# Performance work log

Hardware: AMD Instinct MI355X
Metric: run time of the kernel (lower is better)

The kernel has to match this reference:

```python
import jax, jax.numpy as jnp
import numpy as np
from jax import lax

B, T, H, W, D = 4, 24, 32, 32, 128
N_CONV = 5            # 32 -> 1 via five stride-2 convs
NUM_FREQS = T // 2    # 12
N_EXPERTS = 7         # unique int periods of rfftfreq(24)[1:]
TOP_K = 2
BN_EPS = 1e-5
COMBINE_EPS = float(np.finfo(np.float64).eps)


def setup_inputs() -> dict:
    key = jax.random.key(0)
    ks = jax.random.split(key, 12)
    x = jax.random.normal(ks[0], (B, T, H, W, D), jnp.float32)
    conv_w = jax.random.normal(ks[1], (N_CONV, D, D, 2, 2), jnp.float32) / np.sqrt(4 * D)
    conv_b = jax.random.normal(ks[2], (N_CONV, D), jnp.float32) * 0.1
    bn_gamma = jax.random.uniform(ks[3], (N_CONV, D), jnp.float32, 0.5, 1.5)
    bn_beta = jax.random.normal(ks[4], (N_CONV, D), jnp.float32) * 0.1
    bn_mean = jax.random.normal(ks[5], (N_CONV, D), jnp.float32) * 0.1
    bn_var = jax.random.uniform(ks[6], (N_CONV, D), jnp.float32, 0.5, 1.5)
    fuse_w = jax.random.normal(ks[7], (D, 1), jnp.float32) / np.sqrt(D)
    fuse_b = jax.random.normal(ks[8], (1,), jnp.float32) * 0.1
    w_gate = jax.random.normal(ks[9], (NUM_FREQS, N_EXPERTS), jnp.float32)
    expert_w = jax.random.normal(ks[10], (N_EXPERTS, D, D), jnp.float32) / np.sqrt(D)
    expert_b = jax.random.normal(ks[11], (N_EXPERTS, D), jnp.float32) * 0.1
    return dict(x=x, conv_w=conv_w, conv_b=conv_b, bn_gamma=bn_gamma, bn_beta=bn_beta,
                bn_mean=bn_mean, bn_var=bn_var, fuse_w=fuse_w, fuse_b=fuse_b,
                w_gate=w_gate, expert_w=expert_w, expert_b=expert_b, top_k=TOP_K)


def _gates(x, conv_w, conv_b, bn_gamma, bn_beta, bn_mean, bn_var, fuse_w, fuse_b, w_gate, top_k):
    b, t, h, w, d = x.shape
    # (b t h w d) -> (bt, d, h, w)
    z = jnp.transpose(x.reshape(b * t, h, w, d), (0, 3, 1, 2))
    for i in range(conv_w.shape[0]):  # fixed small layer loop
        z = lax.conv_general_dilated(z, conv_w[i], (2, 2), 'VALID',
                                     dimension_numbers=('NCHW', 'OIHW', 'NCHW'))
        z = z + conv_b[i][None, :, None, None]
        z = bn_gamma[i][None, :, None, None] * (z - bn_mean[i][None, :, None, None]) \
            * lax.rsqrt(bn_var[i][None, :, None, None] + BN_EPS) + bn_beta[i][None, :, None, None]
        z = jnp.where(z > 0, z, 0.2 * z)  # LeakyReLU(0.2)
    hh, ww = z.shape[-2], z.shape[-1]
    # (bt, d, h, w) -> (b, t, h*w*d)  matching einops '(b t) d h w -> b t (h w d)'
    z = jnp.transpose(z.reshape(b, t, d, hh, ww), (0, 1, 3, 4, 2)).reshape(b, t, hh * ww * d)
    s = (z @ fuse_w + fuse_b)[..., 0]  # [B, T]
    xf = jnp.fft.rfft(s, axis=-1, norm='ortho')[:, 1:]  # drop DC -> [B, T//2]
    amp = jnp.abs(xf)
    logits = amp @ w_gate  # [B, E]  (eval path: no noise)
    top_vals, top_idx = lax.top_k(logits, top_k + 1)
    tk_vals, tk_idx = top_vals[:, :top_k], top_idx[:, :top_k]
    tk_gates = jax.nn.softmax(tk_vals, axis=-1)
    gates = jnp.zeros_like(logits).at[jnp.arange(b)[:, None], tk_idx].set(tk_gates)
    return gates


def reference(x, conv_w, conv_b, bn_gamma, bn_beta, bn_mean, bn_var,
              fuse_w, fuse_b, w_gate, expert_w, expert_b, top_k):
    gates = _gates(x, conv_w, conv_b, bn_gamma, bn_beta, bn_mean, bn_var,
                   fuse_w, fuse_b, w_gate, top_k)  # [B, E]
    # Dense equivalent of dispatch -> per-expert linear -> combine:
    # combine does exp(expert_out), gate-weighted scatter-add over batch, then log.
    expert_out = jnp.einsum('bthwd,edf->bethwf', x, expert_w) \
                 + expert_b[None, :, None, None, None, :]  # [B,E,T,H,W,D]
    combined = jnp.einsum('be,bethwf->bthwf', gates, jnp.exp(expert_out))
    combined = jnp.where(combined == 0, COMBINE_EPS, combined)
    return jnp.log(combined)
```

## Files before the change

### kernel.cpp

```cpp
#include <hip/hip_runtime.h>
#include <hip/hip_bf16.h>

#define D_ 128
#define T_ 24
#define NPB 24576
#define TSTR 132

typedef __attribute__((ext_vector_type(8))) short bf16x8;
typedef __attribute__((ext_vector_type(4))) float f32x4;
typedef unsigned short ushortt;

static __device__ __forceinline__ void load8(const float* p, float* dst){
  float4 a = *(const float4*)p; float4 b = *(const float4*)(p+4);
  dst[0]=a.x;dst[1]=a.y;dst[2]=a.z;dst[3]=a.w;dst[4]=b.x;dst[5]=b.y;dst[6]=b.z;dst[7]=b.w;
}
static __device__ __forceinline__ bf16x8 cvt8(const float* f){
  union { bf16x8 v; __hip_bfloat162 h[4]; } u;
#pragma unroll
  for (int i=0;i<4;i++) u.h[i] = __float22bfloat162_rn(make_float2(f[2*i], f[2*i+1]));
  return u.v;
}
static __device__ __forceinline__ void split8(const float* f, bf16x8* hh, bf16x8* ll){
  union { bf16x8 v; __hip_bfloat162 h[4]; } uh, ul;
  float lo[8];
#pragma unroll
  for (int i=0;i<4;i++){
    __hip_bfloat162 p = __float22bfloat162_rn(make_float2(f[2*i], f[2*i+1]));
    uh.h[i] = p;
    lo[2*i]   = f[2*i]   - __bfloat162float(p.x);
    lo[2*i+1] = f[2*i+1] - __bfloat162float(p.y);
  }
#pragma unroll
  for (int i=0;i<4;i++) ul.h[i] = __float22bfloat162_rn(make_float2(lo[2*i], lo[2*i+1]));
  *hh = uh.v; *ll = ul.v;
}

__global__ void prep_frags(const float* __restrict__ cw, const float* __restrict__ ew,
                           ushortt* __restrict__ wfC, ushortt* __restrict__ wfE, int do_e)
{
  const int idx = blockIdx.x*256 + threadIdx.x;
  if (idx < 10240){
    const int l  = idx >> 11;
    const int n  = (idx >> 4) & 127;
    const int k8 = (idx & 15) * 8;
    const float* src = cw + (size_t)((l*128 + n)*128 + k8)*4;
    float4 v[8];
#pragma unroll
    for (int kk=0;kk<8;++kk) v[kk] = *(const float4*)&src[kk*4];
    const int fk = k8>>5, q = (k8>>3)&3, ng = n>>4;
    const int lanoff = (q*16 + (n&15))*8;
#pragma unroll
    for (int tap=0; tap<4; ++tap){
      float f[8];
#pragma unroll
      for (int kk=0;kk<8;++kk) f[kk] = ((const float*)&v[kk])[tap];
      bf16x8 hh, ll; split8(f, &hh, &ll);
      *(bf16x8*)&wfC[(size_t)((((l*4+tap)*2+0)*4+fk)*8+ng)*512 + lanoff] = hh;
      *(bf16x8*)&wfC[(size_t)((((l*4+tap)*2+1)*4+fk)*8+ng)*512 + lanoff] = ll;
    }
  } else if (do_e && idx < 10240 + 14336){
    const int j  = idx - 10240;
    const int e  = j >> 11;
    const int n  = (j >> 4) & 127;
    const int k8 = (j & 15) * 8;
    float f[8];
#pragma unroll
    for (int kk=0;kk<8;++kk) f[kk] = ew[(size_t)(e*128 + k8+kk)*128 + n];
    const int fk = k8>>5, q = (k8>>3)&3, ng = n>>4;
    *(bf16x8*)&wfE[(size_t)((e*4+fk)*8+ng)*512 + (q*16 + (n&15))*8] = cvt8(f);
  }
}

template<int MG>
__global__ __launch_bounds__(256, 4)
void conv3(const float* __restrict__ in, float* __restrict__ out,
           const ushortt* __restrict__ wf,
           const float* __restrict__ cb,  const float* __restrict__ gam,
           const float* __restrict__ bet, const float* __restrict__ mn,
           const float* __restrict__ vr,  int n_pix, int lw)
{
  (void)n_pix;
  const int t = threadIdx.x;
  const int w = t>>6, lane = t&63, quad = lane>>4, l16 = lane&15;
  const int nh = w*32;
  const int row0 = blockIdx.x*(MG*16);
  const int Win = 2<<lw;
  int inb[MG];
#pragma unroll
  for (int mg=0; mg<MG; ++mg){
    const int p = row0 + mg*16 + l16;
    const int n   = p >> (2*lw);
    const int rem = p - (n << (2*lw));
    const int oy  = rem >> lw, ox = rem - (oy<<lw);
    inb[mg] = ((n*Win  + 2*oy)*Win + 2*ox) << 7;
  }
  f32x4 acc[MG][2];
#pragma unroll
  for (int mg=0;mg<MG;++mg){ acc[mg][0]=(f32x4){0,0,0,0}; acc[mg][1]=acc[mg][0]; }

#pragma unroll
  for (int tap=0; tap<4; ++tap){
    const int toff = (((tap>>1)*Win) + (tap&1)) << 7;
#pragma unroll
    for (int fk=0; fk<4; ++fk){
      bf16x8 ah[MG], al[MG];
#pragma unroll
      for (int mg=0; mg<MG; ++mg){
        float f[8]; load8(in + inb[mg] + toff + fk*32 + quad*8, f);
        split8(f, &ah[mg], &al[mg]);
      }
#pragma unroll
      for (int ngl=0; ngl<2; ++ngl){
        const int ng = w*2 + ngl;
        const bf16x8 bh = *(const bf16x8*)&wf[(size_t)(((tap*2+0)*4+fk)*8+ng)*512 + lane*8];
        const bf16x8 bl = *(const bf16x8*)&wf[(size_t)(((tap*2+1)*4+fk)*8+ng)*512 + lane*8];
#pragma unroll
        for (int mg=0; mg<MG; ++mg){
          acc[mg][ngl] = __builtin_amdgcn_mfma_f32_16x16x32_bf16(ah[mg], bh, acc[mg][ngl], 0,0,0);
          acc[mg][ngl] = __builtin_amdgcn_mfma_f32_16x16x32_bf16(ah[mg], bl, acc[mg][ngl], 0,0,0);
          acc[mg][ngl] = __builtin_amdgcn_mfma_f32_16x16x32_bf16(al[mg], bh, acc[mg][ngl], 0,0,0);
        }
      }
    }
  }
#pragma unroll
  for (int ngl=0; ngl<2; ++ngl){
    const int col = nh + ngl*16 + l16;
    const float sc  = gam[col]*rsqrtf(vr[col]+1e-5f);
    const float cbv = cb[col], bt = bet[col], mv = mn[col];
#pragma unroll
    for (int mg=0; mg<MG; ++mg)
#pragma unroll
      for (int r=0; r<4; ++r){
        const int pix = row0 + mg*16 + quad*4 + r;
        float v = acc[mg][ngl][r] + cbv;
        v = sc*(v - mv) + bt;
        out[(size_t)pix*D_ + col] = v>0.f ? v : 0.2f*v;
      }
  }
}

template<int WOUT>
static __device__ __forceinline__ void stage_lds(const float* __restrict__ sIn,
    float* __restrict__ sOut, float* __restrict__ gOut,
    const ushortt* __restrict__ wf,
    const float* __restrict__ cb, const float* __restrict__ gam,
    const float* __restrict__ bet, const float* __restrict__ mn,
    const float* __restrict__ vr, int t)
{
  const int w = t>>6, lane = t&63, quad = lane>>4, l16 = lane&15;
  const int nh = w*32;
  const int R  = WOUT*WOUT;
  const int Wi = 2*WOUT;
  const int p  = (l16 < R) ? l16 : 0;
  const int oy = (WOUT==4) ? (p>>2) : (WOUT==2 ? (p>>1) : 0);
  const int ox = (WOUT==4) ? (p&3)  : (WOUT==2 ? (p&1)  : 0);
  const int inb = 2*oy*Wi + 2*ox;
  f32x4 acc[2];
  acc[0]=(f32x4){0,0,0,0}; acc[1]=acc[0];
#pragma unroll
  for (int tap=0; tap<4; ++tap){
    const int toff = (tap>>1)*Wi + (tap&1);
#pragma unroll
    for (int fk=0; fk<4; ++fk){
      float f[8]; load8(sIn + (size_t)(inb+toff)*TSTR + fk*32 + quad*8, f);
      bf16x8 ah, al; split8(f, &ah, &al);
#pragma unroll
      for (int ngl=0; ngl<2; ++ngl){
        const int ng = w*2 + ngl;
        const bf16x8 bh = *(const bf16x8*)&wf[(size_t)(((tap*2+0)*4+fk)*8+ng)*512 + lane*8];
        const bf16x8 bl = *(const bf16x8*)&wf[(size_t)(((tap*2+1)*4+fk)*8+ng)*512 + lane*8];
        acc[ngl] = __builtin_amdgcn_mfma_f32_16x16x32_bf16(ah, bh, acc[ngl], 0,0,0);
        acc[ngl] = __builtin_amdgcn_mfma_f32_16x16x32_bf16(ah, bl, acc[ngl], 0,0,0);
        acc[ngl] = __builtin_amdgcn_mfma_f32_16x16x32_bf16(al, bh, acc[ngl], 0,0,0);
      }
    }
  }
#pragma unroll
  for (int ngl=0; ngl<2; ++ngl){
    const int col = nh + ngl*16 + l16;
    const float sc  = gam[col]*rsqrtf(vr[col]+1e-5f);
    const float cbv = cb[col], btv = bet[col], mv = mn[col];
#pragma unroll
    for (int r=0; r<4; ++r){
      const int row = quad*4 + r;
      if (row < R){
        float v = acc[ngl][r] + cbv;
        v = sc*(v - mv) + btv;
        v = v>0.f ? v : 0.2f*v;
        if (WOUT > 1) sOut[(size_t)row*TSTR + col] = v;
        else          gOut[col] = v;
      }
    }
  }
}

__global__ __launch_bounds__(256, 2)
void tail_kernel(const float* __restrict__ bufA, const ushortt* __restrict__ wfC,
                 const float* __restrict__ cb,  const float* __restrict__ gam,
                 const float* __restrict__ bet, const float* __restrict__ mn,
                 const float* __restrict__ vr,  float* __restrict__ zbuf)
{
  __shared__ float sA[64*TSTR];
  __shared__ float sB[16*TSTR];
  __shared__ float sC[ 4*TSTR];
  const int bt = blockIdx.x;
  const int t = threadIdx.x;
  const int w = t>>6, lane = t&63, quad = lane>>4, l16 = lane&15;
  const int nh = w*32;

  {
    const ushortt* wf = wfC + 131072;
    int inb[4];
#pragma unroll
    for (int mg=0; mg<4; ++mg){
      const int p = mg*16 + l16;
      const int oy = p>>3, ox = p&7;
      inb[mg] = ((bt*16 + 2*oy)*16 + 2*ox) << 7;
    }
    f32x4 acc[4][2];
#pragma unroll
    for (int mg=0;mg<4;++mg){ acc[mg][0]=(f32x4){0,0,0,0}; acc[mg][1]=acc[mg][0]; }
#pragma unroll
    for (int tap=0; tap<4; ++tap){
      const int toff = (((tap>>1)*16) + (tap&1)) << 7;
#pragma unroll
      for (int fk=0; fk<4; ++fk){
        bf16x8 ah[4], al[4];
#pragma unroll
        for (int mg=0; mg<4; ++mg){
          float f[8]; load8(bufA + (size_t)inb[mg] + toff + fk*32 + quad*8, f);
          split8(f, &ah[mg], &al[mg]);
        }
#pragma unroll
        for (int ngl=0; ngl<2; ++ngl){
          const int ng = w*2 + ngl;
          const bf16x8 bh = *(const bf16x8*)&wf[(size_t)(((tap*2+0)*4+fk)*8+ng)*512 + lane*8];
          const bf16x8 bl = *(const bf16x8*)&wf[(size_t)(((tap*2+1)*4+fk)*8+ng)*512 + lane*8];
#pragma unroll
          for (int mg=0; mg<4; ++mg){
            acc[mg][ngl] = __builtin_amdgcn_mfma_f32_16x16x32_bf16(ah[mg], bh, acc[mg][ngl], 0,0,0);
            acc[mg][ngl] = __builtin_amdgcn_mfma_f32_16x16x32_bf16(ah[mg], bl, acc[mg][ngl], 0,0,0);
            acc[mg][ngl] = __builtin_amdgcn_mfma_f32_16x16x32_bf16(al[mg], bh, acc[mg][ngl], 0,0,0);
          }
        }
      }
    }
#pragma unroll
    for (int ngl=0; ngl<2; ++ngl){
      const int col = nh + ngl*16 + l16;
      const float sc  = gam[128+col]*rsqrtf(vr[128+col]+1e-5f);
      const float cbv = cb[128+col], btv = bet[128+col], mv = mn[128+col];
#pragma unroll
      for (int mg=0; mg<4; ++mg)
#pragma unroll
        for (int r=0; r<4; ++r){
          const int row = mg*16 + quad*4 + r;
          float v = acc[mg][ngl][r] + cbv;
          v = sc*(v - mv) + btv;
          sA[(size_t)row*TSTR + col] = v>0.f ? v : 0.2f*v;
        }
    }
  }
  __syncthreads();
  stage_lds<4>(sA, sB, nullptr, wfC + 262144, cb+256, gam+256, bet+256, mn+256, vr+256, t);
  __syncthreads();
  stage_lds<2>(sB, sC, nullptr, wfC + 393216, cb+384, gam+384, bet+384, mn+384, vr+384, t);
  __syncthreads();
  stage_lds<1>(sC, nullptr, zbuf + (size_t)bt*D_, wfC + 524288, cb+512, gam+512, bet+512, mn+512, vr+512, t);
}

__global__ void gate_kernel(const float* __restrict__ z, const float* __restrict__ fw,
                            const float* __restrict__ fb, const float* __restrict__ wg,
                            float* __restrict__ gbuf)
{
  __shared__ float s[96];
  __shared__ float amp[4][12];
  __shared__ float logits[4][7];
  const int t = threadIdx.x;
  if (t < 96){
    float a = 0.f;
    for (int d=0; d<D_; d++) a = fmaf(z[t*D_+d], fw[d], a);
    s[t] = a + fb[0];
  }
  __syncthreads();
  if (t < 48){
    const int b = t / 12, kf = (t % 12) + 1;
    float re=0.f, im=0.f;
    for (int tt=0; tt<T_; tt++){
      int ph = (kf*tt) % T_;
      float ang = (float)ph * (6.283185307179586f / (float)T_);
      re = fmaf(s[b*T_+tt], cosf(ang), re);
      im = fmaf(s[b*T_+tt], sinf(ang), im);
    }
    amp[b][t%12] = sqrtf(re*re + im*im) * 0.20412414523193150f;
  }
  __syncthreads();
  if (t < 28){
    const int b = t/7, e = t - (t/7)*7;
    float a = 0.f;
    for (int k=0;k<12;k++) a = fmaf(amp[b][k], wg[k*7+e], a);
    logits[b][e] = a;
  }
  __syncthreads();
  if (t < 4){
    const int b = t;
    int i0=0; float v0=logits[b][0];
    for (int e=1;e<7;e++){ float v=logits[b][e]; if (v > v0){ v0=v; i0=e; } }
    int i1=-1; float v1=-3.4e38f;
    for (int e=0;e<7;e++){ if (e==i0) continue; float v=logits[b][e]; if (v > v1){ v1=v; i1=e; } }
    float ed = expf(v1 - v0);
    gbuf[b*4+0] = 1.f/(1.f+ed);
    gbuf[b*4+1] = ed/(1.f+ed);
    ((int*)gbuf)[b*4+2] = i0;
    ((int*)gbuf)[b*4+3] = i1;
  }
}

__global__ __launch_bounds__(256, 3)
void expert_gate(const float* __restrict__ x, const ushortt* __restrict__ wfe,
                 const float* __restrict__ eb, const float* __restrict__ zbuf,
                 const float* __restrict__ fw, const float* __restrict__ fb,
                 const float* __restrict__ wg, float* __restrict__ outp)
{
  __shared__ float ssig[T_];
  __shared__ float samp[12];
  __shared__ float slog[7];
  __shared__ float sg[2];
  __shared__ int   se[2];
  const int t = threadIdx.x;
  const int w = t>>6, lane = t&63, quad = lane>>4, l16 = lane&15;
  const int nh = w*32;
  const size_t row0 = (size_t)blockIdx.x * 64;
  const int b = (int)(row0 / NPB);

  if (t < T_){
    const float* zr = zbuf + (size_t)(b*T_ + t)*D_;
    float a = 0.f;
    for (int d=0; d<D_; d++) a = fmaf(zr[d], fw[d], a);
    ssig[t] = a + fb[0];
  }
  __syncthreads();
  if (t < 12){
    const int kf = t + 1;
    float re=0.f, im=0.f;
    for (int tt=0; tt<T_; tt++){
      int ph = (kf*tt) % T_;
      float ang = (float)ph * (6.283185307179586f / (float)T_);
      re = fmaf(ssig[tt], cosf(ang), re);
      im = fmaf(ssig[tt], sinf(ang), im);
    }
    samp[t] = sqrtf(re*re + im*im) * 0.20412414523193150f;
  }
  __syncthreads();
  if (t < 7){
    float a = 0.f;
    for (int k=0;k<12;k++) a = fmaf(samp[k], wg[k*7+t], a);
    slog[t] = a;
  }
  __syncthreads();
  if (t == 0){
    int i0=0; float v0=slog[0];
    for (int e=1;e<7;e++){ float v=slog[e]; if (v > v0){ v0=v; i0=e; } }
    int i1=-1; float v1=-3.4e38f;
    for (int e=0;e<7;e++){ if (e==i0) continue; float v=slog[e]; if (v > v1){ v1=v; i1=e; } }
    float ed = expf(v1 - v0);
    sg[0] = 1.f/(1.f+ed);
    sg[1] = ed/(1.f+ed);
    se[0] = i0; se[1] = i1;
  }
  __syncthreads();
  const float g0 = sg[0], g1 = sg[1];
  const int e0 = se[0], e1 = se[1];

  f32x4 acc[2][4][2];
#pragma unroll
  for (int e=0;e<2;++e)
#pragma unroll
    for (int mg=0;mg<4;++mg){ acc[e][mg][0]=(f32x4){0,0,0,0}; acc[e][mg][1]=acc[e][mg][0]; }

#pragma unroll
  for (int fk=0; fk<4; ++fk){
    bf16x8 a[4];
#pragma unroll
    for (int mg=0; mg<4; ++mg){
      float f[8]; load8(x + (row0 + mg*16 + l16)*D_ + fk*32 + quad*8, f);
      a[mg] = cvt8(f);
    }
#pragma unroll
    for (int e=0; e<2; ++e){
      const int eg = e ? e1 : e0;
#pragma unroll
      for (int ngl=0; ngl<2; ++ngl){
        const int ng = w*2 + ngl;
        const bf16x8 bb = *(const bf16x8*)&wfe[(size_t)((eg*4+fk)*8+ng)*512 + lane*8];
#pragma unroll
        for (int mg=0; mg<4; ++mg)
          acc[e][mg][ngl] = __builtin_amdgcn_mfma_f32_16x16x32_bf16(a[mg], bb, acc[e][mg][ngl], 0,0,0);
      }
    }
  }
#pragma unroll
  for (int ngl=0; ngl<2; ++ngl){
    const int col = nh + ngl*16 + l16;
    const float be0 = eb[e0*D_ + col];
    const float be1 = eb[e1*D_ + col];
#pragma unroll
    for (int mg=0; mg<4; ++mg)
#pragma unroll
      for (int r=0; r<4; ++r){
        const size_t row = row0 + mg*16 + quad*4 + r;
        float c = g0*__expf(acc[0][mg][ngl][r] + be0) + g1*__expf(acc[1][mg][ngl][r] + be1);
        if (c == 0.f) c = 2.220446049250313e-16f;
        outp[row*D_ + col] = __logf(c);
      }
  }
}

template<bool WF>
__global__ __launch_bounds__(256, 3)
void expert3(const float* __restrict__ x, const float* __restrict__ ew,
             const ushortt* __restrict__ wfe, const float* __restrict__ eb,
             const float* __restrict__ gbuf, float* __restrict__ outp)
{
  __shared__ ushortt wlds[WF ? 16 : 32768];
  const int t = threadIdx.x;
  const int w = t>>6, lane = t&63, quad = lane>>4, l16 = lane&15;
  const int nh = w*32;
  const size_t row0 = (size_t)blockIdx.x * 64;
  const int b = (int)(row0 / NPB);
  const float g0 = gbuf[b*4+0], g1 = gbuf[b*4+1];
  const int e0 = ((const int*)gbuf)[b*4+2];
  const int e1 = ((const int*)gbuf)[b*4+3];

  if (!WF){
    const int el = t>>7, r7 = t&127;
    const int n0 = (r7&31)*4, k0 = (r7>>5)*16;
    const int esel = el ? e1 : e0;
#pragma unroll
    for (int h=0; h<2; ++h)
#pragma unroll
      for (int sub=0; sub<2; ++sub){
        const int kb = h*64 + k0 + sub*8;
        float4 v[8];
#pragma unroll
        for (int kk=0;kk<8;++kk)
          v[kk] = *(const float4*)&ew[(size_t)esel*16384 + (size_t)(kb+kk)*D_ + n0];
        const int fk = kb>>5, q = (kb>>3)&3;
#pragma unroll
        for (int n=0;n<4;++n){
          float f[8];
#pragma unroll
          for (int kk=0;kk<8;++kk) f[kk] = ((const float*)&v[kk])[n];
          *(bf16x8*)&wlds[(size_t)(((el*4+fk)*8 + ((n0+n)>>4))*512 + (q*16 + ((n0+n)&15))*8)] = cvt8(f);
        }
      }
    __syncthreads();
  }

  f32x4 acc[2][4][2];
#pragma unroll
  for (int e=0;e<2;++e)
#pragma unroll
    for (int mg=0;mg<4;++mg){ acc[e][mg][0]=(f32x4){0,0,0,0}; acc[e][mg][1]=acc[e][mg][0]; }

#pragma unroll
  for (int fk=0; fk<4; ++fk){
    bf16x8 a[4];
#pragma unroll
    for (int mg=0; mg<4; ++mg){
      float f[8]; load8(x + (row0 + mg*16 + l16)*D_ + fk*32 + quad*8, f);
      a[mg] = cvt8(f);
    }
#pragma unroll
    for (int e=0; e<2; ++e){
      const int eg = e ? e1 : e0;
#pragma unroll
      for (int ngl=0; ngl<2; ++ngl){
        const int ng = w*2 + ngl;
        bf16x8 bb;
        if (WF) bb = *(const bf16x8*)&wfe[(size_t)((eg*4+fk)*8+ng)*512 + lane*8];
        else    bb = *(const bf16x8*)&wlds[(size_t)((e*4+fk)*8+ng)*512 + lane*8];
#pragma unroll
        for (int mg=0; mg<4; ++mg)
          acc[e][mg][ngl] = __builtin_amdgcn_mfma_f32_16x16x32_bf16(a[mg], bb, acc[e][mg][ngl], 0,0,0);
      }
    }
  }
#pragma unroll
  for (int ngl=0; ngl<2; ++ngl){
    const int col = nh + ngl*16 + l16;
    const float be0 = eb[e0*D_ + col];
    const float be1 = eb[e1*D_ + col];
#pragma unroll
    for (int mg=0; mg<4; ++mg)
#pragma unroll
      for (int r=0; r<4; ++r){
        const size_t row = row0 + mg*16 + quad*4 + r;
        float c = g0*__expf(acc[0][mg][ngl][r] + be0) + g1*__expf(acc[1][mg][ngl][r] + be1);
        if (c == 0.f) c = 2.220446049250313e-16f;
        outp[row*D_ + col] = __logf(c);
      }
  }
}

extern "C" void kernel_launch(void* const* d_in, const int* in_sizes, int n_in,
                              void* d_out, int out_size, void* d_ws, size_t ws_size,
                              hipStream_t stream)
{
  const float* x   = (const float*)d_in[0];
  const float* cw  = (const float*)d_in[1];
  const float* cb  = (const float*)d_in[2];
  const float* gam = (const float*)d_in[3];
  const float* bet = (const float*)d_in[4];
  const float* mn  = (const float*)d_in[5];
  const float* vr  = (const float*)d_in[6];
  const float* fw  = (const float*)d_in[7];
  const float* fb  = (const float*)d_in[8];
  const float* wg  = (const float*)d_in[9];
  const float* ew  = (const float*)d_in[10];
  const float* eb  = (const float*)d_in[11];
  float* out = (float*)d_out;

  char* sb = (char*)d_out;
  ushortt* wfC = (ushortt*)sb;
  float* bufA  = (float*)(sb + 1310720);

  const size_t WFE_BYTES = (size_t)7*4*8*512*2;
  const bool primary = ws_size >= WFE_BYTES + 96*D_*sizeof(float);
  ushortt* wfE = (ushortt*)d_ws;
  float* zbuf_ws = (float*)((char*)d_ws + WFE_BYTES);

  if (primary){
    prep_frags<<<96, 256, 0, stream>>>(cw, ew, wfC, wfE, 1);
    conv3<2><<<768, 256, 0, stream>>>(x, bufA, wfC, cb, gam, bet, mn, vr, 24576, 4);
    tail_kernel<<<96, 256, 0, stream>>>(bufA, wfC, cb, gam, bet, mn, vr, zbuf_ws);
    expert_gate<<<1536, 256, 0, stream>>>(x, wfE, eb, zbuf_ws, fw, fb, wg, out);
    return;
  }

  float* bufB  = (float*)(sb + 13893632);
  float* zbuf  = (float*)(sb + 17039360);
  float* gbuf  = (float*)d_ws;
  const bool use_wf = ws_size >= (size_t)(64 + WFE_BYTES);
  ushortt* wfE2 = use_wf ? (ushortt*)((char*)d_ws + 64) : wfC;

  prep_frags<<<96, 256, 0, stream>>>(cw, ew, wfC, wfE2, use_wf ? 1 : 0);
  conv3<2><<<768, 256, 0, stream>>>(x,    bufA, wfC,          cb,     gam,     bet,     mn,     vr,     24576, 4);
  conv3<2><<<192, 256, 0, stream>>>(bufA, bufB, wfC + 131072, cb+128, gam+128, bet+128, mn+128, vr+128,  6144, 3);
  conv3<1><<< 96, 256, 0, stream>>>(bufB, bufA, wfC + 262144, cb+256, gam+256, bet+256, mn+256, vr+256,  1536, 2);
  conv3<1><<< 24, 256, 0, stream>>>(bufA, bufB, wfC + 393216, cb+384, gam+384, bet+384, mn+384, vr+384,   384, 1);
  conv3<1><<<  6, 256, 0, stream>>>(bufB, zbuf, wfC + 524288, cb+512, gam+512, bet+512, mn+512, vr+512,    96, 0);
  gate_kernel<<<1, 128, 0, stream>>>(zbuf, fw, fb, wg, gbuf);
  if (use_wf) expert3<true ><<<1536, 256, 0, stream>>>(x, ew, wfE2, eb, gbuf, out);
  else        expert3<false><<<1536, 256, 0, stream>>>(x, ew, wfE2, eb, gbuf, out);
}
```

Measured before the change: 223.1 us.

## Hoist gating into separate kernel and use logsumexp combine in expert kernel

Gate computation (fuse projection, DFT, top-k softmax) is taken out of every expert block and run once in a single-block gate_kernel. The expert kernel now reads precomputed gates, processes two 64-row tiles per block with half the grid, and raises the occupancy hint. The exp/sum/log combine is rewritten as a stable log-sum-exp with log-gates folded into the bias, cutting transcendental calls. The trade-off is one extra tiny kernel launch on the serial path, and the epsilon clamp for an exact-zero sum is dropped.

New measurement: 244.8 us. 9.7% more time.

```diff
diff --git a/kernel.cpp b/kernel.cpp
--- a/kernel.cpp
+++ b/kernel.cpp
@@ -317,103 +317,67 @@
   }
 }
 
-__global__ __launch_bounds__(256, 3)
-void expert_gate(const float* __restrict__ x, const ushortt* __restrict__ wfe,
-                 const float* __restrict__ eb, const float* __restrict__ zbuf,
-                 const float* __restrict__ fw, const float* __restrict__ fb,
-                 const float* __restrict__ wg, float* __restrict__ outp)
-{
-  __shared__ float ssig[T_];
-  __shared__ float samp[12];
-  __shared__ float slog[7];
-  __shared__ float sg[2];
-  __shared__ int   se[2];
+__global__ __launch_bounds__(256, 4)
+void expert_lse(const float* __restrict__ x, const ushortt* __restrict__ wfe,
+                const float* __restrict__ eb, const float* __restrict__ gbuf,
+                float* __restrict__ outp)
+{
   const int t = threadIdx.x;
   const int w = t>>6, lane = t&63, quad = lane>>4, l16 = lane&15;
   const int nh = w*32;
-  const size_t row0 = (size_t)blockIdx.x * 64;
-  const int b = (int)(row0 / NPB);
-
-  if (t < T_){
-    const float* zr = zbuf + (size_t)(b*T_ + t)*D_;
-    float a = 0.f;
-    for (int d=0; d<D_; d++) a = fmaf(zr[d], fw[d], a);
-    ssig[t] = a + fb[0];
-  }
-  __syncthreads();
-  if (t < 12){
-    const int kf = t + 1;
-    float re=0.f, im=0.f;
-    for (int tt=0; tt<T_; tt++){
-      int ph = (kf*tt) % T_;
-      float ang = (float)ph * (6.283185307179586f / (float)T_);
-      re = fmaf(ssig[tt], cosf(ang), re);
-      im = fmaf(ssig[tt], sinf(ang), im);
-    }
-    samp[t] = sqrtf(re*re + im*im) * 0.20412414523193150f;
-  }
-  __syncthreads();
-  if (t < 7){
-    float a = 0.f;
-    for (int k=0;k<12;k++) a = fmaf(samp[k], wg[k*7+t], a);
-    slog[t] = a;
-  }
-  __syncthreads();
-  if (t == 0){
-    int i0=0; float v0=slog[0];
-    for (int e=1;e<7;e++){ float v=slog[e]; if (v > v0){ v0=v; i0=e; } }
-    int i1=-1; float v1=-3.4e38f;
-    for (int e=0;e<7;e++){ if (e==i0) continue; float v=slog[e]; if (v > v1){ v1=v; i1=e; } }
-    float ed = expf(v1 - v0);
-    sg[0] = 1.f/(1.f+ed);
-    sg[1] = ed/(1.f+ed);
-    se[0] = i0; se[1] = i1;
-  }
-  __syncthreads();
-  const float g0 = sg[0], g1 = sg[1];
-  const int e0 = se[0], e1 = se[1];
-
-  f32x4 acc[2][4][2];
-#pragma unroll
-  for (int e=0;e<2;++e)
-#pragma unroll
-    for (int mg=0;mg<4;++mg){ acc[e][mg][0]=(f32x4){0,0,0,0}; acc[e][mg][1]=acc[e][mg][0]; }
-
-#pragma unroll
-  for (int fk=0; fk<4; ++fk){
-    bf16x8 a[4];
-#pragma unroll
-    for (int mg=0; mg<4; ++mg){
-      float f[8]; load8(x + (row0 + mg*16 + l16)*D_ + fk*32 + quad*8, f);
-      a[mg] = cvt8(f);
-    }
-#pragma unroll
-    for (int e=0; e<2; ++e){
-      const int eg = e ? e1 : e0;
-#pragma unroll
-      for (int ngl=0; ngl<2; ++ngl){
-        const int ng = w*2 + ngl;
-        const bf16x8 bb = *(const bf16x8*)&wfe[(size_t)((eg*4+fk)*8+ng)*512 + lane*8];
-#pragma unroll
-        for (int mg=0; mg<4; ++mg)
-          acc[e][mg][ngl] = __builtin_amdgcn_mfma_f32_16x16x32_bf16(a[mg], bb, acc[e][mg][ngl], 0,0,0);
-      }
-    }
-  }
-#pragma unroll
-  for (int ngl=0; ngl<2; ++ngl){
-    const int col = nh + ngl*16 + l16;
-    const float be0 = eb[e0*D_ + col];
-    const float be1 = eb[e1*D_ + col];
-#pragma unroll
-    for (int mg=0; mg<4; ++mg)
-#pragma unroll
-      for (int r=0; r<4; ++r){
-        const size_t row = row0 + mg*16 + quad*4 + r;
-        float c = g0*__expf(acc[0][mg][ngl][r] + be0) + g1*__expf(acc[1][mg][ngl][r] + be1);
-        if (c == 0.f) c = 2.220446049250313e-16f;
-        outp[row*D_ + col] = __logf(c);
-      }
+
+#pragma unroll
+  for (int tile=0; tile<2; ++tile){
+    const size_t row0 = (size_t)(blockIdx.x + tile*768) * 64;
+    const int b = (int)(row0 / NPB);
+    const float g0 = gbuf[b*4+0], g1 = gbuf[b*4+1];
+    const int e0 = ((const int*)gbuf)[b*4+2];
+    const int e1 = ((const int*)gbuf)[b*4+3];
+    const float lg0 = __logf(g0), lg1 = __logf(g1);
+
+    f32x4 acc[2][4][2];
+#pragma unroll
+    for (int e=0;e<2;++e)
+#pragma unroll
+      for (int mg=0;mg<4;++mg){ acc[e][mg][0]=(f32x4){0,0,0,0}; acc[e][mg][1]=acc[e][mg][0]; }
+
+#pragma unroll
+    for (int fk=0; fk<4; ++fk){
+      bf16x8 a[4];
+#pragma unroll
+      for (int mg=0; mg<4; ++mg){
+        float f[8]; load8(x + (row0 + mg*16 + l16)*D_ + fk*32 + quad*8, f);
+        a[mg] = cvt8(f);
+      }
+#pragma unroll
+      for (int e=0; e<2; ++e){
+        const int eg = e ? e1 : e0;
+#pragma unroll
+        for (int ngl=0; ngl<2; ++ngl){
+          const int ng = w*2 + ngl;
+          const bf16x8 bb = *(const bf16x8*)&wfe[(size_t)((eg*4+fk)*8+ng)*512 + lane*8];
+#pragma unroll
+          for (int mg=0; mg<4; ++mg)
+            acc[e][mg][ngl] = __builtin_amdgcn_mfma_f32_16x16x32_bf16(a[mg], bb, acc[e][mg][ngl], 0,0,0);
+        }
+      }
+    }
+#pragma unroll
+    for (int ngl=0; ngl<2; ++ngl){
+      const int col = nh + ngl*16 + l16;
+      const float be0 = eb[e0*D_ + col] + lg0;
+      const float be1 = eb[e1*D_ + col] + lg1;
+#pragma unroll
+      for (int mg=0; mg<4; ++mg)
+#pragma unroll
+        for (int r=0; r<4; ++r){
+          const size_t row = row0 + mg*16 + quad*4 + r;
+          const float u = acc[0][mg][ngl][r] + be0;
+          const float v = acc[1][mg][ngl][r] + be1;
+          const float m = fmaxf(u, v);
+          outp[row*D_ + col] = m + __logf(1.f + __expf(-fabsf(u - v)));
+        }
+    }
   }
 }
 
@@ -527,15 +491,18 @@
   float* bufA  = (float*)(sb + 1310720);
 
   const size_t WFE_BYTES = (size_t)7*4*8*512*2;
-  const bool primary = ws_size >= WFE_BYTES + 96*D_*sizeof(float);
+  const size_t ZB_BYTES  = (size_t)96*D_*sizeof(float);
+  const bool primary = ws_size >= WFE_BYTES + ZB_BYTES + 64;
   ushortt* wfE = (ushortt*)d_ws;
   float* zbuf_ws = (float*)((char*)d_ws + WFE_BYTES);
+  float* gbuf_ws = (float*)((char*)d_ws + WFE_BYTES + ZB_BYTES);
 
   if (primary){
     prep_frags<<<96, 256, 0, stream>>>(cw, ew, wfC, wfE, 1);
     conv3<2><<<768, 256, 0, stream>>>(x, bufA, wfC, cb, gam, bet, mn, vr, 24576, 4);
     tail_kernel<<<96, 256, 0, stream>>>(bufA, wfC, cb, gam, bet, mn, vr, zbuf_ws);
-    expert_gate<<<1536, 256, 0, stream>>>(x, wfE, eb, zbuf_ws, fw, fb, wg, out);
+    gate_kernel<<<1, 128, 0, stream>>>(zbuf_ws, fw, fb, wg, gbuf_ws);
+    expert_lse<<<768, 256, 0, stream>>>(x, wfE, eb, gbuf_ws, out);
     return;
   }
 
```
